# Kernel optimization log

Hardware: AMD Instinct MI355X
Metric: run time of the kernel (lower is better)

Reference implementation:

```python
import jax, jax.numpy as jnp
import numpy as np

N, E, D, C, H1 = 50000, 800000, 128, 8, 2


def setup_inputs() -> dict:
    key = jax.random.key(0)
    ks = jax.random.split(key, 14)
    s = lambda k, sh: (jax.random.normal(k, sh, jnp.float32) * 0.05)
    return {
        "x": jax.random.normal(ks[0], (N, D), jnp.float32),
        "edge_index": jax.random.randint(ks[1], (2, E), 0, N, dtype=jnp.int32),
        # conv1: GATConv(D, D, heads=2, concat=True)
        "W1": s(ks[2], (D, H1 * D)),
        "att1_src": s(ks[3], (H1, D)),
        "att1_dst": s(ks[4], (H1, D)),
        "b1": s(ks[5], (H1 * D,)),
        # conv2: GATConv(2D, D, heads=1, concat=False)
        "W2": s(ks[6], (H1 * D, D)),
        "att2_src": s(ks[7], (1, D)),
        "att2_dst": s(ks[8], (1, D)),
        "b2": s(ks[9], (D,)),
        # MLP head
        "Wm1": s(ks[10], (D, D)),
        "bm1": s(ks[11], (D,)),
        "Wm2": s(ks[12], (D, C)),
        "bm2": s(ks[13], (C,)),
    }


def gat_conv(x, src, dst, W, a_src, a_dst, b, heads, out_ch, concat):
    """PyG GATConv (eval mode): self-loops added by caller, softmax over
    edges grouped by destination node, negative_slope=0.2."""
    n = x.shape[0]
    h = (x @ W).reshape(n, heads, out_ch)              # [N,H,F]
    alpha_src = jnp.einsum('nhf,hf->nh', h, a_src)     # [N,H]
    alpha_dst = jnp.einsum('nhf,hf->nh', h, a_dst)     # [N,H]
    e = jax.nn.leaky_relu(alpha_src[src] + alpha_dst[dst], 0.2)  # [E,H]
    e_max = jax.ops.segment_max(e, dst, num_segments=n)
    ex = jnp.exp(e - e_max[dst])
    denom = jax.ops.segment_sum(ex, dst, num_segments=n)
    alpha = ex / jnp.maximum(denom[dst], 1e-16)        # [E,H]
    out = jax.ops.segment_sum(h[src] * alpha[:, :, None], dst, num_segments=n)
    out = out.reshape(n, heads * out_ch) if concat else out.mean(axis=1)
    return out + b


def reference(x, edge_index, W1, att1_src, att1_dst, b1,
              W2, att2_src, att2_dst, b2, Wm1, bm1, Wm2, bm2):
    n = x.shape[0]
    loop = jnp.arange(n, dtype=edge_index.dtype)
    src = jnp.concatenate([edge_index[0], loop])  # add_self_loops=True
    dst = jnp.concatenate([edge_index[1], loop])
    h = jax.nn.elu(gat_conv(x, src, dst, W1, att1_src, att1_dst, b1, H1, D, True))
    h = jax.nn.elu(gat_conv(h, src, dst, W2, att2_src, att2_dst, b2, 1, D, False))
    h = jax.nn.relu(h @ Wm1 + bm1)
    return jax.nn.relu(h @ Wm2 + bm2)
```

## Files before the change

### kernel.cpp

```cpp
#include <hip/hip_runtime.h>
#include <hip/hip_bf16.h>


__device__ __forceinline__ float lrelu(float x){ return x > 0.f ? x : 0.2f*x; }
__device__ __forceinline__ float elu_f(float x){ return x > 0.f ? x : __expf(x) - 1.f; }
__device__ __forceinline__ unsigned short f2bf(float f){
  __hip_bfloat16 h = __float2bfloat16(f);
  return *reinterpret_cast<unsigned short*>(&h);
}
__device__ __forceinline__ float bflo(unsigned int u){ return __uint_as_float(u << 16); }
__device__ __forceinline__ float bfhi(unsigned int u){ return __uint_as_float(u & 0xffff0000u); }
__device__ __forceinline__ unsigned int packbf(float a, float b){
  return (unsigned int)f2bf(a) | ((unsigned int)f2bf(b) << 16);
}

typedef __attribute__((ext_vector_type(8))) short bf16x8;
typedef __attribute__((ext_vector_type(4))) float f32x4;

__global__ void prep_kernel(const float* __restrict__ W1, unsigned short* __restrict__ BT1a,
                            unsigned short* __restrict__ BT1b,
                            const float* __restrict__ W2, unsigned short* __restrict__ BT2,
                            const float* __restrict__ Wm1, unsigned short* __restrict__ BT3,
                            const float* __restrict__ a1s, const float* __restrict__ a1d,
                            float* __restrict__ va, int* __restrict__ bcount,
                            int* __restrict__ gcur, int NB){
  int idx = blockIdx.x*256 + threadIdx.x;
  const int S1 = 128*256, S2 = 128*256, S3 = 128*128;
  if (idx < S1){
    int k = idx >> 8, c = idx & 255;
    unsigned short v = f2bf(W1[idx]);
    if (c < 128) BT1a[c*128 + k] = v;
    else         BT1b[(c-128)*128 + k] = v;
  } else if (idx < S1 + S2){
    int j = idx - S1;
    int k = j >> 7, n = j & 127;
    BT2[n*256 + k] = f2bf(W2[j]);
  } else if (idx < S1 + S2 + S3){
    int j = idx - S1 - S2;
    int k = j >> 7, n = j & 127;
    BT3[n*128 + k] = f2bf(Wm1[j]);
  } else if (idx < S1 + S2 + S3 + 512){
    int j = idx - S1 - S2 - S3;
    int v = j >> 7, k = j & 127;
    const float* avec = (v < 2) ? a1s : a1d;
    int head = v & 1;
    const float4* wrow = (const float4*)(W1 + (size_t)k*256 + head*128);
    const float4* arow = (const float4*)(avec + head*128);
    float s = 0.f;
    #pragma unroll 8
    for (int f = 0; f < 32; ++f){
      float4 w = wrow[f], a = arow[f];
      s += w.x*a.x + w.y*a.y + w.z*a.z + w.w*a.w;
    }
    va[j] = s;
  } else if (idx < S1 + S2 + S3 + 512 + 2048){
    int z = idx - (S1 + S2 + S3 + 512);
    if (z < 1024){ if (z < NB) bcount[z] = 0; }
    else { z -= 1024; if (z < NB) gcur[z] = 0; }
  }
}

__global__ __launch_bounds__(256) void f2bf_hist_kernel(
    const float* __restrict__ x, unsigned short* __restrict__ xb, int N,
    const float* __restrict__ va, float* __restrict__ as1, float* __restrict__ ad1,
    const int* __restrict__ dst, int E, int* __restrict__ bcount, int NB, int nbConv)
{
  __shared__ int h[1024];
  if ((int)blockIdx.x < nbConv){
    int i = blockIdx.x*256 + threadIdx.x;
    int total = N*32;
    float4 v = make_float4(0.f,0.f,0.f,0.f);
    if (i < total){
      v = ((const float4*)x)[i];
      ushort4 u; u.x=f2bf(v.x); u.y=f2bf(v.y); u.z=f2bf(v.z); u.w=f2bf(v.w);
      ((ushort4*)xb)[i] = u;
    }
    int c = (i & 31) << 2;
    float4 vs0 = *(const float4*)(va + c);
    float4 vs1 = *(const float4*)(va + 128 + c);
    float4 vd0 = *(const float4*)(va + 256 + c);
    float4 vd1 = *(const float4*)(va + 384 + c);
    float s0 = v.x*vs0.x + v.y*vs0.y + v.z*vs0.z + v.w*vs0.w;
    float s1 = v.x*vs1.x + v.y*vs1.y + v.z*vs1.z + v.w*vs1.w;
    float d0 = v.x*vd0.x + v.y*vd0.y + v.z*vd0.z + v.w*vd0.w;
    float d1 = v.x*vd1.x + v.y*vd1.y + v.z*vd1.z + v.w*vd1.w;
    #pragma unroll
    for (int m = 1; m <= 16; m <<= 1){
      s0 += __shfl_xor(s0, m); s1 += __shfl_xor(s1, m);
      d0 += __shfl_xor(d0, m); d1 += __shfl_xor(d1, m);
    }
    if ((i & 31) == 0 && i < total){
      int n = i >> 5;
      *(float2*)(as1 + 2*n) = make_float2(s0, s1);
      *(float2*)(ad1 + 2*n) = make_float2(d0, d1);
    }
  } else {
    for (int i = threadIdx.x; i < NB; i += 256) h[i] = 0;
    __syncthreads();
    int b0 = blockIdx.x - nbConv;
    for (int e = b0*256 + threadIdx.x; e < E; e += 64*256)
      atomicAdd(&h[dst[e] >> 6], 1);
    __syncthreads();
    for (int i = threadIdx.x; i < NB; i += 256)
      if (h[i]) atomicAdd(&bcount[i], h[i]);
  }
}

__global__ __launch_bounds__(256) void bscatter_kernel(
    const int* __restrict__ src, const int* __restrict__ dst, int E,
    const int* __restrict__ bcount, int* __restrict__ boff,
    int* __restrict__ gcur, unsigned int* __restrict__ pairs, int NB)
{
  __shared__ int h[1024];
  __shared__ int runbase[1024];
  __shared__ int sc[1024];
  const int t = threadIdx.x;
  const int e0 = blockIdx.x * 4096;

  for (int i = t; i < 1024; i += 256) sc[i] = (i < NB) ? bcount[i] : 0;
  for (int i = t; i < NB; i += 256) h[i] = 0;
  __syncthreads();
  for (int d = 1; d < 1024; d <<= 1){
    int v0 = (t       >= d) ? sc[t       - d] : 0;
    int v1 = (t + 256 >= d) ? sc[t + 256 - d] : 0;
    int v2 = (t + 512 >= d) ? sc[t + 512 - d] : 0;
    int v3 = (t + 768 >= d) ? sc[t + 768 - d] : 0;
    __syncthreads();
    sc[t] += v0; sc[t+256] += v1; sc[t+512] += v2; sc[t+768] += v3;
    __syncthreads();
  }
  if (blockIdx.x == 0){
    for (int i = t; i <= NB; i += 256) boff[i] = i ? sc[i-1] : 0;
  }

  int myb[16]; unsigned int myw[16];
  #pragma unroll
  for (int q = 0; q < 16; ++q){
    int e = e0 + q*256 + t;
    int b = -1; unsigned int w = 0;
    if (e < E){
      int d = dst[e];
      b = d >> 6;
      w = ((unsigned int)(d & 63) << 26) | (unsigned int)src[e];
      atomicAdd(&h[b], 1);
    }
    myb[q] = b; myw[q] = w;
  }
  __syncthreads();
  for (int i = t; i < NB; i += 256)
    runbase[i] = h[i] ? atomicAdd(&gcur[i], h[i]) : 0;
  __syncthreads();
  for (int i = t; i < NB; i += 256) h[i] = 0;
  __syncthreads();
  #pragma unroll
  for (int q = 0; q < 16; ++q){
    if (myb[q] >= 0){
      int off = atomicAdd(&h[myb[q]], 1);
      int base = myb[q] ? sc[myb[q]-1] : 0;
      pairs[(size_t)base + runbase[myb[q]] + off] = myw[q];
    }
  }
}

__global__ __launch_bounds__(256) void bbuild_kernel(
    const unsigned int* __restrict__ pairs, const int* __restrict__ boff,
    int* __restrict__ rowptr, int* __restrict__ csr, int N)
{
  __shared__ int deg[64], offs[64], cur[64];
  const int b = blockIdx.x;
  const int t = threadIdx.x;
  const int n0 = b << 6;
  const int nNodes = min(64, N - n0);
  const int p0 = boff[b], p1 = boff[b+1];
  const int base = p0 + n0;
  if (t < 64) deg[t] = (t < nNodes) ? 1 : 0;
  __syncthreads();
  for (int i = p0 + t; i < p1; i += 256)
    atomicAdd(&deg[pairs[i] >> 26], 1);
  __syncthreads();
  if (t < 64){
    int x = deg[t];
    #pragma unroll
    for (int d = 1; d < 64; d <<= 1){
      int y = __shfl_up(x, d);
      if (t >= d) x += y;
    }
    offs[t] = x - deg[t];
    cur[t] = 1;
    if (t < nNodes){
      rowptr[n0 + t + 1] = base + x;
      csr[base + x - deg[t]] = n0 + t;
    }
    if (b == 0 && t == 0) rowptr[0] = 0;
  }
  __syncthreads();
  for (int i = p0 + t; i < p1; i += 256){
    unsigned int w = pairs[i];
    int dl = w >> 26;
    int s  = (int)(w & 0x03ffffffu);
    int off = atomicAdd(&cur[dl], 1);
    csr[base + offs[dl] + off] = s;
  }
}

__device__ __forceinline__ void gemm_core(
    const unsigned short* __restrict__ A, int lda,
    const unsigned short* __restrict__ BT, int M, int K, int r0,
    unsigned short* a_s, unsigned short* b_s, f32x4 (&acc)[4][4])
{
  const int tid  = threadIdx.x;
  const int lane = tid & 63, wv = tid >> 6;
  const int mh = (wv & 1)*64, nh = (wv >> 1)*64;
  const int l15 = lane & 15, quad = lane >> 4;
  const int srow = tid >> 3, skc = tid & 7;

  #pragma unroll
  for (int i = 0; i < 4; ++i)
    #pragma unroll
    for (int j = 0; j < 4; ++j)
      #pragma unroll
      for (int r = 0; r < 4; ++r) acc[i][j][r] = 0.f;

  for (int k0 = 0; k0 < K; k0 += 64){
    #pragma unroll
    for (int it = 0; it < 4; ++it){
      int row = it*32 + srow;
      int grow = r0 + row;
      uint4 v = make_uint4(0u,0u,0u,0u);
      if (grow < M) v = *(const uint4*)(A + (size_t)grow*lda + k0 + skc*8);
      *(uint4*)(&a_s[row*72 + skc*8]) = v;
    }
    #pragma unroll
    for (int it = 0; it < 4; ++it){
      int row = it*32 + srow;
      uint4 v = *(const uint4*)(BT + (size_t)row*K + k0 + skc*8);
      *(uint4*)(&b_s[row*72 + skc*8]) = v;
    }
    __syncthreads();
    #pragma unroll
    for (int ks = 0; ks < 64; ks += 32){
      bf16x8 af[4], bfr[4];
      #pragma unroll
      for (int i = 0; i < 4; ++i)
        af[i] = *(const bf16x8*)(&a_s[(mh + i*16 + l15)*72 + ks + quad*8]);
      #pragma unroll
      for (int j = 0; j < 4; ++j)
        bfr[j] = *(const bf16x8*)(&b_s[(nh + j*16 + l15)*72 + ks + quad*8]);
      #pragma unroll
      for (int i = 0; i < 4; ++i)
        #pragma unroll
        for (int j = 0; j < 4; ++j)
          acc[i][j] = __builtin_amdgcn_mfma_f32_16x16x32_bf16(bfr[j], af[i], acc[i][j], 0, 0, 0);
    }
    __syncthreads();
  }
}

__global__ __launch_bounds__(256) void gemm_conv2_kernel(
    const unsigned short* __restrict__ out1b, const unsigned short* __restrict__ BT2,
    unsigned short* __restrict__ h2b, int M,
    const float* __restrict__ a2s, const float* __restrict__ a2d,
    float* __restrict__ as2, float* __restrict__ ad2)
{
  __shared__ unsigned short a_s[128*72];
  __shared__ unsigned short b_s[128*72];
  __shared__ float part_s[128][2];
  __shared__ float part_d[128][2];
  const int r0 = blockIdx.y*128;
  f32x4 acc[4][4];
  gemm_core(out1b, 256, BT2, M, 256, r0, a_s, b_s, acc);

  const int tid = threadIdx.x;
  const int lane = tid & 63, wv = tid >> 6;
  const int mh = (wv & 1)*64, nh = (wv >> 1)*64;
  const int l15 = lane & 15, quad = lane >> 4;
  #pragma unroll
  for (int i = 0; i < 4; ++i){
    int m = r0 + mh + i*16 + l15;
    float ps = 0.f, pd = 0.f;
    #pragma unroll
    for (int j = 0; j < 4; ++j){
      int n = nh + j*16 + quad*4;
      float4 wsv = *(const float4*)(a2s + n);
      float4 wdv = *(const float4*)(a2d + n);
      float v0 = acc[i][j][0], v1 = acc[i][j][1], v2 = acc[i][j][2], v3 = acc[i][j][3];
      ps += v0*wsv.x + v1*wsv.y + v2*wsv.z + v3*wsv.w;
      pd += v0*wdv.x + v1*wdv.y + v2*wdv.z + v3*wdv.w;
      if (m < M){
        ushort4 u;
        u.x = f2bf(v0); u.y = f2bf(v1); u.z = f2bf(v2); u.w = f2bf(v3);
        *(ushort4*)(h2b + (size_t)m*128 + n) = u;
      }
    }
    ps += __shfl_xor(ps, 16); ps += __shfl_xor(ps, 32);
    pd += __shfl_xor(pd, 16); pd += __shfl_xor(pd, 32);
    if (quad == 0){
      part_s[mh + i*16 + l15][wv >> 1] = ps;
      part_d[mh + i*16 + l15][wv >> 1] = pd;
    }
  }
  __syncthreads();
  if (tid < 128){
    int gm = r0 + tid;
    if (gm < M){
      as2[gm] = part_s[tid][0] + part_s[tid][1];
      ad2[gm] = part_d[tid][0] + part_d[tid][1];
    }
  }
}

#define AGG1_FMA(u, a0v, a1v) do{ \
    float f0 = bflo(u.x), f1 = bfhi(u.x), f2v = bflo(u.y), f3 = bfhi(u.y); \
    float f4 = bflo(u.z), f5 = bfhi(u.z), f6 = bflo(u.w), f7 = bfhi(u.w); \
    acc0[0] += a0v*f0; acc0[1] += a0v*f1; acc0[2] += a0v*f2v; acc0[3] += a0v*f3; \
    acc0[4] += a0v*f4; acc0[5] += a0v*f5; acc0[6] += a0v*f6;  acc0[7] += a0v*f7; \
    acc1[0] += a1v*f0; acc1[1] += a1v*f1; acc1[2] += a1v*f2v; acc1[3] += a1v*f3; \
    acc1[4] += a1v*f4; acc1[5] += a1v*f5; acc1[6] += a1v*f6;  acc1[7] += a1v*f7; \
  }while(0)

#define AGG2_FMA(u, av) do{ \
    acc[0] += av*bflo(u.x); acc[1] += av*bfhi(u.x); \
    acc[2] += av*bflo(u.y); acc[3] += av*bfhi(u.y); \
    acc[4] += av*bflo(u.z); acc[5] += av*bfhi(u.z); \
    acc[6] += av*bflo(u.w); acc[7] += av*bfhi(u.w); \
  }while(0)

__global__ __launch_bounds__(256, 4) void agg1gemm_kernel(
    const unsigned short* __restrict__ xb, const float* __restrict__ as_,
    const float* __restrict__ ad_, const int* __restrict__ rowptr, const int* __restrict__ csr,
    const unsigned short* __restrict__ BT1a, const unsigned short* __restrict__ BT1b,
    const float* __restrict__ b1, unsigned short* __restrict__ out1b, int N)
{
  __shared__ unsigned short xa_s[16*264];
  const int tid = threadIdx.x;
  const int wv = tid >> 6, lane = tid & 63;
  const int ql = lane & 15;
  const int g = wv*4 + (lane >> 4);
  const int n = blockIdx.x*16 + g;
  const bool valid = n < N;
  int start = 0, end = 0;
  float2 adv = make_float2(0.f, 0.f);
  if (valid){ start = rowptr[n]; end = rowptr[n+1]; adv = *(const float2*)(ad_ + 2*n); }

  int jl = start + ql;
  bool have = valid && (jl < end);
  int s_l = 0;
  float p0 = 0.f, p1 = 0.f;
  if (have){
    s_l = csr[jl];
    float2 av = *(const float2*)(as_ + 2*s_l);
    p0 = __expf(lrelu(av.x + adv.x));
    p1 = __expf(lrelu(av.y + adv.y));
  }
  float l0 = p0, l1 = p1;
  for (int j = jl + 16; j < end; j += 16){
    int s = csr[j];
    float2 av = *(const float2*)(as_ + 2*s);
    l0 += __expf(lrelu(av.x + adv.x));
    l1 += __expf(lrelu(av.y + adv.y));
  }
  #pragma unroll
  for (int msk = 1; msk <= 8; msk <<= 1){
    l0 += __shfl_xor(l0, msk);
    l1 += __shfl_xor(l1, msk);
  }
  float inv0 = 1.f / fmaxf(l0, 1e-16f);
  float inv1 = 1.f / fmaxf(l1, 1e-16f);
  float a0_l = p0 * inv0;
  float a1_l = p1 * inv1;

  float acc0[8], acc1[8];
  #pragma unroll
  for (int i = 0; i < 8; ++i){ acc0[i] = 0.f; acc1[i] = 0.f; }
  const int c = ql << 3;
  const unsigned short* hp = xb + c;

  #pragma unroll
  for (int t = 0; t < 16; t += 2){
    int   sA  = __shfl(s_l, t, 16),   sB  = __shfl(s_l, t+1, 16);
    float a0A = __shfl(a0_l, t, 16),  a0B = __shfl(a0_l, t+1, 16);
    float a1A = __shfl(a1_l, t, 16),  a1B = __shfl(a1_l, t+1, 16);
    uint4 uA = *(const uint4*)(hp + (sA << 7));
    uint4 uB = *(const uint4*)(hp + (sB << 7));
    AGG1_FMA(uA, a0A, a1A);
    AGG1_FMA(uB, a0B, a1B);
  }
  for (int jb = start + 16; jb < end; jb += 16){
    int jl2 = jb + ql;
    int s2 = 0; float a0_2 = 0.f, a1_2 = 0.f;
    if (jl2 < end){
      s2 = csr[jl2];
      float2 av = *(const float2*)(as_ + 2*s2);
      a0_2 = __expf(lrelu(av.x + adv.x)) * inv0;
      a1_2 = __expf(lrelu(av.y + adv.y)) * inv1;
    }
    int cnt2 = min(16, end - jb);
    for (int t2 = 0; t2 < cnt2; t2 += 2){
      int   sA  = __shfl(s2, t2, 16),   sB  = __shfl(s2, t2+1, 16);
      float a0A = __shfl(a0_2, t2, 16), a0B = __shfl(a0_2, t2+1, 16);
      float a1A = __shfl(a1_2, t2, 16), a1B = __shfl(a1_2, t2+1, 16);
      uint4 uA = *(const uint4*)(hp + (sA << 7));
      uint4 uB = *(const uint4*)(hp + (sB << 7));
      AGG1_FMA(uA, a0A, a1A);
      AGG1_FMA(uB, a0B, a1B);
    }
  }

  {
    uint4 u0, u1;
    u0.x = packbf(acc0[0], acc0[1]); u0.y = packbf(acc0[2], acc0[3]);
    u0.z = packbf(acc0[4], acc0[5]); u0.w = packbf(acc0[6], acc0[7]);
    u1.x = packbf(acc1[0], acc1[1]); u1.y = packbf(acc1[2], acc1[3]);
    u1.z = packbf(acc1[4], acc1[5]); u1.w = packbf(acc1[6], acc1[7]);
    *(uint4*)(&xa_s[g*264 + c])       = u0;
    *(uint4*)(&xa_s[g*264 + 128 + c]) = u1;
  }
  __syncthreads();

  const int h = wv >> 1;
  const int colbase = (wv & 1)*64;
  const unsigned short* BT = (h ? BT1b : BT1a) + (size_t)colbase*128;
  const int l15 = lane & 15, quad = lane >> 4;
  f32x4 acc[4];
  #pragma unroll
  for (int j = 0; j < 4; ++j)
    #pragma unroll
    for (int r = 0; r < 4; ++r) acc[j][r] = 0.f;

  #pragma unroll
  for (int ks = 0; ks < 128; ks += 32){
    bf16x8 af = *(const bf16x8*)(&xa_s[l15*264 + h*128 + ks + quad*8]);
    #pragma unroll
    for (int j = 0; j < 4; ++j){
      bf16x8 bfr = *(const bf16x8*)(BT + (size_t)(j*16 + l15)*128 + ks + quad*8);
      acc[j] = __builtin_amdgcn_mfma_f32_16x16x32_bf16(bfr, af, acc[j], 0, 0, 0);
    }
  }

  const int m = blockIdx.x*16 + l15;
  if (m < N){
    const float* bias = b1 + h*128 + colbase;
    #pragma unroll
    for (int j = 0; j < 4; ++j){
      int nn = j*16 + quad*4;
      float4 bb = *(const float4*)(bias + nn);
      ushort4 u;
      u.x = f2bf(elu_f(acc[j][0] + bb.x));
      u.y = f2bf(elu_f(acc[j][1] + bb.y));
      u.z = f2bf(elu_f(acc[j][2] + bb.z));
      u.w = f2bf(elu_f(acc[j][3] + bb.w));
      *(ushort4*)(out1b + (size_t)m*256 + h*128 + colbase + nn) = u;
    }
  }
}

__global__ __launch_bounds__(256, 4) void agg2mlp_kernel(
    const unsigned short* __restrict__ h2b, const float* __restrict__ as_,
    const float* __restrict__ ad_, const int* __restrict__ rowptr, const int* __restrict__ csr,
    const float* __restrict__ b2, const unsigned short* __restrict__ BT3,
    const float* __restrict__ bm1, const float* __restrict__ Wm2,
    const float* __restrict__ bm2, float* __restrict__ out, int N)
{
  __shared__ unsigned short gb_s[16*136];
  __shared__ float wm2_s[128*8];
  __shared__ float part[16][4][8];
  const int tid = threadIdx.x;
  {
    int i4 = tid*4;
    *(float4*)(&wm2_s[i4]) = *(const float4*)(Wm2 + i4);
  }
  const int wv = tid >> 6, lane = tid & 63;
  const int ql = lane & 15;
  const int g = wv*4 + (lane >> 4);
  const int n = blockIdx.x*16 + g;
  const bool valid = n < N;
  int start = 0, end = 0;
  float adn = 0.f;
  if (valid){ start = rowptr[n]; end = rowptr[n+1]; adn = ad_[n]; }

  int jl = start + ql;
  bool have = valid && (jl < end);
  int s_l = 0;
  float p_l = 0.f;
  if (have){
    s_l = csr[jl];
    p_l = __expf(lrelu(as_[s_l] + adn));
  }
  float l = p_l;
  for (int j = jl + 16; j < end; j += 16)
    l += __expf(lrelu(as_[csr[j]] + adn));
  #pragma unroll
  for (int msk = 1; msk <= 8; msk <<= 1) l += __shfl_xor(l, msk);
  float inv = 1.f / fmaxf(l, 1e-16f);
  float a_l = p_l * inv;

  float acc[8];
  #pragma unroll
  for (int i = 0; i < 8; ++i) acc[i] = 0.f;
  const int c = ql << 3;
  const unsigned short* hp = h2b + c;

  #pragma unroll
  for (int t = 0; t < 16; t += 2){
    int   sA = __shfl(s_l, t, 16),  sB = __shfl(s_l, t+1, 16);
    float aA = __shfl(a_l, t, 16),  aB = __shfl(a_l, t+1, 16);
    uint4 uA = *(const uint4*)(hp + (sA << 7));
    uint4 uB = *(const uint4*)(hp + (sB << 7));
    AGG2_FMA(uA, aA);
    AGG2_FMA(uB, aB);
  }
  for (int jb = start + 16; jb < end; jb += 16){
    int jl2 = jb + ql;
    int s2 = 0; float a2 = 0.f;
    if (jl2 < end){
      s2 = csr[jl2];
      a2 = __expf(lrelu(as_[s2] + adn)) * inv;
    }
    int cnt2 = min(16, end - jb);
    for (int t2 = 0; t2 < cnt2; t2 += 2){
      int   sA = __shfl(s2, t2, 16),  sB = __shfl(s2, t2+1, 16);
      float aA = __shfl(a2, t2, 16),  aB = __shfl(a2, t2+1, 16);
      uint4 uA = *(const uint4*)(hp + (sA << 7));
      uint4 uB = *(const uint4*)(hp + (sB << 7));
      AGG2_FMA(uA, aA);
      AGG2_FMA(uB, aB);
    }
  }

  {
    float4 bb0 = *(const float4*)(b2 + c);
    float4 bb1 = *(const float4*)(b2 + c + 4);
    float o[8];
    o[0]=elu_f(acc[0]+bb0.x); o[1]=elu_f(acc[1]+bb0.y);
    o[2]=elu_f(acc[2]+bb0.z); o[3]=elu_f(acc[3]+bb0.w);
    o[4]=elu_f(acc[4]+bb1.x); o[5]=elu_f(acc[5]+bb1.y);
    o[6]=elu_f(acc[6]+bb1.z); o[7]=elu_f(acc[7]+bb1.w);
    uint4 up;
    up.x = packbf(o[0], o[1]); up.y = packbf(o[2], o[3]);
    up.z = packbf(o[4], o[5]); up.w = packbf(o[6], o[7]);
    *(uint4*)(&gb_s[g*136 + c]) = up;
  }
  __syncthreads();

  const int l15 = lane & 15, quad = lane >> 4;
  const int nh = wv*32;
  f32x4 macc[2];
  #pragma unroll
  for (int j = 0; j < 2; ++j)
    #pragma unroll
    for (int r = 0; r < 4; ++r) macc[j][r] = 0.f;

  #pragma unroll
  for (int ks = 0; ks < 128; ks += 32){
    bf16x8 af = *(const bf16x8*)(&gb_s[l15*136 + ks + quad*8]);
    #pragma unroll
    for (int j = 0; j < 2; ++j){
      bf16x8 bfr = *(const bf16x8*)(BT3 + (size_t)(nh + j*16 + l15)*128 + ks + quad*8);
      macc[j] = __builtin_amdgcn_mfma_f32_16x16x32_bf16(bfr, af, macc[j], 0, 0, 0);
    }
  }

  float po[8];
  #pragma unroll
  for (int o = 0; o < 8; ++o) po[o] = 0.f;
  #pragma unroll
  for (int j = 0; j < 2; ++j){
    int nn = nh + j*16 + quad*4;
    float4 bb = *(const float4*)(bm1 + nn);
    #pragma unroll
    for (int r = 0; r < 4; ++r){
      float hcol = fmaxf(macc[j][r] + ((const float*)&bb)[r], 0.f);
      const float* wr = &wm2_s[(nn + r)*8];
      #pragma unroll
      for (int o = 0; o < 8; ++o) po[o] += hcol*wr[o];
    }
  }
  #pragma unroll
  for (int o = 0; o < 8; ++o){
    po[o] += __shfl_xor(po[o], 16);
    po[o] += __shfl_xor(po[o], 32);
  }
  if (quad == 0){
    #pragma unroll
    for (int o = 0; o < 8; ++o) part[l15][wv][o] = po[o];
  }
  __syncthreads();
  if (tid < 16){
    int gm = blockIdx.x*16 + tid;
    if (gm < N){
      float4 o0, o1;
      o0.x = fmaxf(part[tid][0][0]+part[tid][1][0]+part[tid][2][0]+part[tid][3][0] + bm2[0], 0.f);
      o0.y = fmaxf(part[tid][0][1]+part[tid][1][1]+part[tid][2][1]+part[tid][3][1] + bm2[1], 0.f);
      o0.z = fmaxf(part[tid][0][2]+part[tid][1][2]+part[tid][2][2]+part[tid][3][2] + bm2[2], 0.f);
      o0.w = fmaxf(part[tid][0][3]+part[tid][1][3]+part[tid][2][3]+part[tid][3][3] + bm2[3], 0.f);
      o1.x = fmaxf(part[tid][0][4]+part[tid][1][4]+part[tid][2][4]+part[tid][3][4] + bm2[4], 0.f);
      o1.y = fmaxf(part[tid][0][5]+part[tid][1][5]+part[tid][2][5]+part[tid][3][5] + bm2[5], 0.f);
      o1.z = fmaxf(part[tid][0][6]+part[tid][1][6]+part[tid][2][6]+part[tid][3][6] + bm2[6], 0.f);
      o1.w = fmaxf(part[tid][0][7]+part[tid][1][7]+part[tid][2][7]+part[tid][3][7] + bm2[7], 0.f);
      *(float4*)(out + (size_t)gm*8)     = o0;
      *(float4*)(out + (size_t)gm*8 + 4) = o1;
    }
  }
}

extern "C" void kernel_launch(void* const* d_in, const int* in_sizes, int n_in,
                              void* d_out, int out_size, void* d_ws, size_t ws_size,
                              hipStream_t stream)
{
  (void)n_in; (void)out_size; (void)ws_size;
  const float* x   = (const float*)d_in[0];
  const int*   ei  = (const int*)d_in[1];
  const float* W1  = (const float*)d_in[2];
  const float* a1s = (const float*)d_in[3];
  const float* a1d = (const float*)d_in[4];
  const float* b1  = (const float*)d_in[5];
  const float* W2  = (const float*)d_in[6];
  const float* a2s = (const float*)d_in[7];
  const float* a2d = (const float*)d_in[8];
  const float* b2  = (const float*)d_in[9];
  const float* Wm1 = (const float*)d_in[10];
  const float* bm1 = (const float*)d_in[11];
  const float* Wm2 = (const float*)d_in[12];
  const float* bm2 = (const float*)d_in[13];
  float* out = (float*)d_out;

  const int N = in_sizes[0] / 128;
  const int E = in_sizes[1] / 2;
  const int NB = (N + 63) >> 6;
  const int* srcp = ei;
  const int* dstp = ei + E;

  char* ws = (char*)d_ws;
  unsigned short* xb    = (unsigned short*)ws;
  unsigned short* out1b = (unsigned short*)(ws + (size_t)N*256);
  unsigned short* h2b   = (unsigned short*)(ws + (size_t)N*768);
  char* tail = ws + (size_t)N*1024;
  unsigned short* BT1a = (unsigned short*)tail;
  unsigned short* BT1b = BT1a + 128*128;
  unsigned short* BT2  = BT1b + 128*128;
  unsigned short* BT3  = BT2 + 128*256;
  float* va   = (float*)(BT3 + 128*128);
  float* as1  = va + 512;
  float* ad1  = as1 + (size_t)2*N;
  float* as2  = ad1 + (size_t)2*N;
  float* ad2  = as2 + N;
  int* bcount = (int*)(ad2 + N);
  int* boff   = bcount + 1024;
  int* gcur   = boff + 1032;
  int* rowptr = gcur + 1024;
  int* csr    = rowptr + N + 1;
  unsigned int* pairs = (unsigned int*)(csr + E + N);

  const int nbConv = (N*32 + 255)/256;
  const int prepTotal = 128*256 + 128*256 + 128*128 + 512 + 2048;

  prep_kernel<<<(prepTotal + 255)/256, 256, 0, stream>>>(
      W1, BT1a, BT1b, W2, BT2, Wm1, BT3, a1s, a1d, va, bcount, gcur, NB);
  f2bf_hist_kernel<<<nbConv + 64, 256, 0, stream>>>(x, xb, N, va, as1, ad1,
                                                    dstp, E, bcount, NB, nbConv);
  bscatter_kernel<<<(E + 4095)/4096, 256, 0, stream>>>(srcp, dstp, E, bcount, boff, gcur, pairs, NB);
  bbuild_kernel<<<NB, 256, 0, stream>>>(pairs, boff, rowptr, csr, N);

  const int nb16 = (N + 15) / 16;
  const int gy   = (N + 127) / 128;

  agg1gemm_kernel<<<nb16, 256, 0, stream>>>(xb, as1, ad1, rowptr, csr,
                                            BT1a, BT1b, b1, out1b, N);
  gemm_conv2_kernel<<<dim3(1, gy), 256, 0, stream>>>(out1b, BT2, h2b, N, a2s, a2d, as2, ad2);
  agg2mlp_kernel<<<nb16, 256, 0, stream>>>(h2b, as2, ad2, rowptr, csr,
                                           b2, BT3, bm1, Wm2, bm2, out, N);
}
```

Baseline: 267.1 us.

## Make aggregation+GEMM per-wave independent, removing block barriers

Both fused aggregation kernels now give each wave its own 8 nodes, processed in two passes, and a private LDS tile, so each wave runs its MFMA GEMM without a block-wide __syncthreads. Each block covers 32 nodes instead of 16, and the second kernel drops its cross-wave partial-sum reduction through shared memory. The cost is that half of the 16 MFMA rows are wasted and each wave now loads the full weight matrix instead of a slice, which raises weight traffic and MFMA work per node.

```diff
diff --git a/kernel.cpp b/kernel.cpp
--- a/kernel.cpp
+++ b/kernel.cpp
@@ -331,125 +331,127 @@
     const unsigned short* __restrict__ BT1a, const unsigned short* __restrict__ BT1b,
     const float* __restrict__ b1, unsigned short* __restrict__ out1b, int N)
 {
-  __shared__ unsigned short xa_s[16*264];
+  __shared__ unsigned short xa_s[4][8*264];
   const int tid = threadIdx.x;
   const int wv = tid >> 6, lane = tid & 63;
   const int ql = lane & 15;
-  const int g = wv*4 + (lane >> 4);
-  const int n = blockIdx.x*16 + g;
-  const bool valid = n < N;
-  int start = 0, end = 0;
-  float2 adv = make_float2(0.f, 0.f);
-  if (valid){ start = rowptr[n]; end = rowptr[n+1]; adv = *(const float2*)(ad_ + 2*n); }
-
-  int jl = start + ql;
-  bool have = valid && (jl < end);
-  int s_l = 0;
-  float p0 = 0.f, p1 = 0.f;
-  if (have){
-    s_l = csr[jl];
-    float2 av = *(const float2*)(as_ + 2*s_l);
-    p0 = __expf(lrelu(av.x + adv.x));
-    p1 = __expf(lrelu(av.y + adv.y));
-  }
-  float l0 = p0, l1 = p1;
-  for (int j = jl + 16; j < end; j += 16){
-    int s = csr[j];
-    float2 av = *(const float2*)(as_ + 2*s);
-    l0 += __expf(lrelu(av.x + adv.x));
-    l1 += __expf(lrelu(av.y + adv.y));
-  }
-  #pragma unroll
-  for (int msk = 1; msk <= 8; msk <<= 1){
-    l0 += __shfl_xor(l0, msk);
-    l1 += __shfl_xor(l1, msk);
-  }
-  float inv0 = 1.f / fmaxf(l0, 1e-16f);
-  float inv1 = 1.f / fmaxf(l1, 1e-16f);
-  float a0_l = p0 * inv0;
-  float a1_l = p1 * inv1;
-
-  float acc0[8], acc1[8];
-  #pragma unroll
-  for (int i = 0; i < 8; ++i){ acc0[i] = 0.f; acc1[i] = 0.f; }
   const int c = ql << 3;
   const unsigned short* hp = xb + c;
-
-  #pragma unroll
-  for (int t = 0; t < 16; t += 2){
-    int   sA  = __shfl(s_l, t, 16),   sB  = __shfl(s_l, t+1, 16);
-    float a0A = __shfl(a0_l, t, 16),  a0B = __shfl(a0_l, t+1, 16);
-    float a1A = __shfl(a1_l, t, 16),  a1B = __shfl(a1_l, t+1, 16);
-    uint4 uA = *(const uint4*)(hp + (sA << 7));
-    uint4 uB = *(const uint4*)(hp + (sB << 7));
-    AGG1_FMA(uA, a0A, a1A);
-    AGG1_FMA(uB, a0B, a1B);
-  }
-  for (int jb = start + 16; jb < end; jb += 16){
-    int jl2 = jb + ql;
-    int s2 = 0; float a0_2 = 0.f, a1_2 = 0.f;
-    if (jl2 < end){
-      s2 = csr[jl2];
-      float2 av = *(const float2*)(as_ + 2*s2);
-      a0_2 = __expf(lrelu(av.x + adv.x)) * inv0;
-      a1_2 = __expf(lrelu(av.y + adv.y)) * inv1;
-    }
-    int cnt2 = min(16, end - jb);
-    for (int t2 = 0; t2 < cnt2; t2 += 2){
-      int   sA  = __shfl(s2, t2, 16),   sB  = __shfl(s2, t2+1, 16);
-      float a0A = __shfl(a0_2, t2, 16), a0B = __shfl(a0_2, t2+1, 16);
-      float a1A = __shfl(a1_2, t2, 16), a1B = __shfl(a1_2, t2+1, 16);
+  unsigned short* xs = &xa_s[wv][0];
+  const int nodebase = blockIdx.x*32 + wv*8;
+
+  for (int pass = 0; pass < 2; ++pass){
+    const int row = pass*4 + (lane >> 4);
+    const int n = nodebase + row;
+    const bool valid = n < N;
+    int start = 0, end = 0;
+    float2 adv = make_float2(0.f, 0.f);
+    if (valid){ start = rowptr[n]; end = rowptr[n+1]; adv = *(const float2*)(ad_ + 2*n); }
+
+    int jl = start + ql;
+    bool have = valid && (jl < end);
+    int s_l = 0;
+    float p0 = 0.f, p1 = 0.f;
+    if (have){
+      s_l = csr[jl];
+      float2 av = *(const float2*)(as_ + 2*s_l);
+      p0 = __expf(lrelu(av.x + adv.x));
+      p1 = __expf(lrelu(av.y + adv.y));
+    }
+    float l0 = p0, l1 = p1;
+    for (int j = jl + 16; j < end; j += 16){
+      int s = csr[j];
+      float2 av = *(const float2*)(as_ + 2*s);
+      l0 += __expf(lrelu(av.x + adv.x));
+      l1 += __expf(lrelu(av.y + adv.y));
+    }
+    #pragma unroll
+    for (int msk = 1; msk <= 8; msk <<= 1){
+      l0 += __shfl_xor(l0, msk);
+      l1 += __shfl_xor(l1, msk);
+    }
+    float inv0 = 1.f / fmaxf(l0, 1e-16f);
+    float inv1 = 1.f / fmaxf(l1, 1e-16f);
+    float a0_l = p0 * inv0;
+    float a1_l = p1 * inv1;
+
+    float acc0[8], acc1[8];
+    #pragma unroll
+    for (int i = 0; i < 8; ++i){ acc0[i] = 0.f; acc1[i] = 0.f; }
+
+    #pragma unroll
+    for (int t = 0; t < 16; t += 2){
+      int   sA  = __shfl(s_l, t, 16),   sB  = __shfl(s_l, t+1, 16);
+      float a0A = __shfl(a0_l, t, 16),  a0B = __shfl(a0_l, t+1, 16);
+      float a1A = __shfl(a1_l, t, 16),  a1B = __shfl(a1_l, t+1, 16);
       uint4 uA = *(const uint4*)(hp + (sA << 7));
       uint4 uB = *(const uint4*)(hp + (sB << 7));
       AGG1_FMA(uA, a0A, a1A);
       AGG1_FMA(uB, a0B, a1B);
     }
-  }
-
-  {
+    for (int jb = start + 16; jb < end; jb += 16){
+      int jl2 = jb + ql;
+      int s2 = 0; float a0_2 = 0.f, a1_2 = 0.f;
+      if (jl2 < end){
+        s2 = csr[jl2];
+        float2 av = *(const float2*)(as_ + 2*s2);
+        a0_2 = __expf(lrelu(av.x + adv.x)) * inv0;
+        a1_2 = __expf(lrelu(av.y + adv.y)) * inv1;
+      }
+      int cnt2 = min(16, end - jb);
+      for (int t2 = 0; t2 < cnt2; t2 += 2){
+        int   sA  = __shfl(s2, t2, 16),   sB  = __shfl(s2, t2+1, 16);
+        float a0A = __shfl(a0_2, t2, 16), a0B = __shfl(a0_2, t2+1, 16);
+        float a1A = __shfl(a1_2, t2, 16), a1B = __shfl(a1_2, t2+1, 16);
+        uint4 uA = *(const uint4*)(hp + (sA << 7));
+        uint4 uB = *(const uint4*)(hp + (sB << 7));
+        AGG1_FMA(uA, a0A, a1A);
+        AGG1_FMA(uB, a0B, a1B);
+      }
+    }
+
     uint4 u0, u1;
     u0.x = packbf(acc0[0], acc0[1]); u0.y = packbf(acc0[2], acc0[3]);
     u0.z = packbf(acc0[4], acc0[5]); u0.w = packbf(acc0[6], acc0[7]);
     u1.x = packbf(acc1[0], acc1[1]); u1.y = packbf(acc1[2], acc1[3]);
     u1.z = packbf(acc1[4], acc1[5]); u1.w = packbf(acc1[6], acc1[7]);
-    *(uint4*)(&xa_s[g*264 + c])       = u0;
-    *(uint4*)(&xa_s[g*264 + 128 + c]) = u1;
-  }
-  __syncthreads();
-
-  const int h = wv >> 1;
-  const int colbase = (wv & 1)*64;
-  const unsigned short* BT = (h ? BT1b : BT1a) + (size_t)colbase*128;
+    *(uint4*)(&xs[row*264 + c])       = u0;
+    *(uint4*)(&xs[row*264 + 128 + c]) = u1;
+  }
+  asm volatile("" ::: "memory");
+
   const int l15 = lane & 15, quad = lane >> 4;
-  f32x4 acc[4];
-  #pragma unroll
-  for (int j = 0; j < 4; ++j)
-    #pragma unroll
-    for (int r = 0; r < 4; ++r) acc[j][r] = 0.f;
-
-  #pragma unroll
-  for (int ks = 0; ks < 128; ks += 32){
-    bf16x8 af = *(const bf16x8*)(&xa_s[l15*264 + h*128 + ks + quad*8]);
-    #pragma unroll
-    for (int j = 0; j < 4; ++j){
-      bf16x8 bfr = *(const bf16x8*)(BT + (size_t)(j*16 + l15)*128 + ks + quad*8);
-      acc[j] = __builtin_amdgcn_mfma_f32_16x16x32_bf16(bfr, af, acc[j], 0, 0, 0);
-    }
-  }
-
-  const int m = blockIdx.x*16 + l15;
-  if (m < N){
-    const float* bias = b1 + h*128 + colbase;
-    #pragma unroll
-    for (int j = 0; j < 4; ++j){
-      int nn = j*16 + quad*4;
-      float4 bb = *(const float4*)(bias + nn);
-      ushort4 u;
-      u.x = f2bf(elu_f(acc[j][0] + bb.x));
-      u.y = f2bf(elu_f(acc[j][1] + bb.y));
-      u.z = f2bf(elu_f(acc[j][2] + bb.z));
-      u.w = f2bf(elu_f(acc[j][3] + bb.w));
-      *(ushort4*)(out1b + (size_t)m*256 + h*128 + colbase + nn) = u;
+  const int arow = l15 & 7;
+  const int m = nodebase + l15;
+  const bool mok = (l15 < 8) && (m < N);
+  #pragma unroll
+  for (int h = 0; h < 2; ++h){
+    bf16x8 af[4];
+    #pragma unroll
+    for (int k = 0; k < 4; ++k)
+      af[k] = *(const bf16x8*)(&xs[arow*264 + h*128 + k*32 + quad*8]);
+    const unsigned short* BT = h ? BT1b : BT1a;
+    const float* bias = b1 + h*128;
+    #pragma unroll
+    for (int j = 0; j < 8; ++j){
+      f32x4 acc;
+      #pragma unroll
+      for (int r = 0; r < 4; ++r) acc[r] = 0.f;
+      #pragma unroll
+      for (int k = 0; k < 4; ++k){
+        bf16x8 bfr = *(const bf16x8*)(BT + (size_t)(j*16 + l15)*128 + k*32 + quad*8);
+        acc = __builtin_amdgcn_mfma_f32_16x16x32_bf16(bfr, af[k], acc, 0, 0, 0);
+      }
+      if (mok){
+        int nn = j*16 + quad*4;
+        float4 bb = *(const float4*)(bias + nn);
+        ushort4 u;
+        u.x = f2bf(elu_f(acc[0] + bb.x));
+        u.y = f2bf(elu_f(acc[1] + bb.y));
+        u.z = f2bf(elu_f(acc[2] + bb.z));
+        u.w = f2bf(elu_f(acc[3] + bb.w));
+        *(ushort4*)(out1b + (size_t)m*256 + h*128 + nn) = u;
+      }
     }
   }
 }
@@ -461,73 +463,77 @@
     const float* __restrict__ bm1, const float* __restrict__ Wm2,
     const float* __restrict__ bm2, float* __restrict__ out, int N)
 {
-  __shared__ unsigned short gb_s[16*136];
+  __shared__ unsigned short gb_s[4][8*136];
   __shared__ float wm2_s[128*8];
-  __shared__ float part[16][4][8];
   const int tid = threadIdx.x;
   {
     int i4 = tid*4;
     *(float4*)(&wm2_s[i4]) = *(const float4*)(Wm2 + i4);
   }
+  __syncthreads();
+
   const int wv = tid >> 6, lane = tid & 63;
   const int ql = lane & 15;
-  const int g = wv*4 + (lane >> 4);
-  const int n = blockIdx.x*16 + g;
-  const bool valid = n < N;
-  int start = 0, end = 0;
-  float adn = 0.f;
-  if (valid){ start = rowptr[n]; end = rowptr[n+1]; adn = ad_[n]; }
-
-  int jl = start + ql;
-  bool have = valid && (jl < end);
-  int s_l = 0;
-  float p_l = 0.f;
-  if (have){
-    s_l = csr[jl];
-    p_l = __expf(lrelu(as_[s_l] + adn));
-  }
-  float l = p_l;
-  for (int j = jl + 16; j < end; j += 16)
-    l += __expf(lrelu(as_[csr[j]] + adn));
-  #pragma unroll
-  for (int msk = 1; msk <= 8; msk <<= 1) l += __shfl_xor(l, msk);
-  float inv = 1.f / fmaxf(l, 1e-16f);
-  float a_l = p_l * inv;
-
-  float acc[8];
-  #pragma unroll
-  for (int i = 0; i < 8; ++i) acc[i] = 0.f;
   const int c = ql << 3;
   const unsigned short* hp = h2b + c;
-
-  #pragma unroll
-  for (int t = 0; t < 16; t += 2){
-    int   sA = __shfl(s_l, t, 16),  sB = __shfl(s_l, t+1, 16);
-    float aA = __shfl(a_l, t, 16),  aB = __shfl(a_l, t+1, 16);
-    uint4 uA = *(const uint4*)(hp + (sA << 7));
-    uint4 uB = *(const uint4*)(hp + (sB << 7));
-    AGG2_FMA(uA, aA);
-    AGG2_FMA(uB, aB);
-  }
-  for (int jb = start + 16; jb < end; jb += 16){
-    int jl2 = jb + ql;
-    int s2 = 0; float a2 = 0.f;
-    if (jl2 < end){
-      s2 = csr[jl2];
-      a2 = __expf(lrelu(as_[s2] + adn)) * inv;
-    }
-    int cnt2 = min(16, end - jb);
-    for (int t2 = 0; t2 < cnt2; t2 += 2){
-      int   sA = __shfl(s2, t2, 16),  sB = __shfl(s2, t2+1, 16);
-      float aA = __shfl(a2, t2, 16),  aB = __shfl(a2, t2+1, 16);
+  unsigned short* gs = &gb_s[wv][0];
+  const int nodebase = blockIdx.x*32 + wv*8;
+
+  for (int pass = 0; pass < 2; ++pass){
+    const int row = pass*4 + (lane >> 4);
+    const int n = nodebase + row;
+    const bool valid = n < N;
+    int start = 0, end = 0;
+    float adn = 0.f;
+    if (valid){ start = rowptr[n]; end = rowptr[n+1]; adn = ad_[n]; }
+
+    int jl = start + ql;
+    bool have = valid && (jl < end);
+    int s_l = 0;
+    float p_l = 0.f;
+    if (have){
+      s_l = csr[jl];
+      p_l = __expf(lrelu(as_[s_l] + adn));
+    }
+    float l = p_l;
+    for (int j = jl + 16; j < end; j += 16)
+      l += __expf(lrelu(as_[csr[j]] + adn));
+    #pragma unroll
+    for (int msk = 1; msk <= 8; msk <<= 1) l += __shfl_xor(l, msk);
+    float inv = 1.f / fmaxf(l, 1e-16f);
+    float a_l = p_l * inv;
+
+    float acc[8];
+    #pragma unroll
+    for (int i = 0; i < 8; ++i) acc[i] = 0.f;
+
+    #pragma unroll
+    for (int t = 0; t < 16; t += 2){
+      int   sA = __shfl(s_l, t, 16),  sB = __shfl(s_l, t+1, 16);
+      float aA = __shfl(a_l, t, 16),  aB = __shfl(a_l, t+1, 16);
       uint4 uA = *(const uint4*)(hp + (sA << 7));
       uint4 uB = *(const uint4*)(hp + (sB << 7));
       AGG2_FMA(uA, aA);
       AGG2_FMA(uB, aB);
     }
-  }
-
-  {
+    for (int jb = start + 16; jb < end; jb += 16){
+      int jl2 = jb + ql;
+      int s2 = 0; float a2 = 0.f;
+      if (jl2 < end){
+        s2 = csr[jl2];
+        a2 = __expf(lrelu(as_[s2] + adn)) * inv;
+      }
+      int cnt2 = min(16, end - jb);
+      for (int t2 = 0; t2 < cnt2; t2 += 2){
+        int   sA = __shfl(s2, t2, 16),  sB = __shfl(s2, t2+1, 16);
+        float aA = __shfl(a2, t2, 16),  aB = __shfl(a2, t2+1, 16);
+        uint4 uA = *(const uint4*)(hp + (sA << 7));
+        uint4 uB = *(const uint4*)(hp + (sB << 7));
+        AGG2_FMA(uA, aA);
+        AGG2_FMA(uB, aB);
+      }
+    }
+
     float4 bb0 = *(const float4*)(b2 + c);
     float4 bb1 = *(const float4*)(b2 + c + 4);
     float o[8];
@@ -538,38 +544,35 @@
     uint4 up;
     up.x = packbf(o[0], o[1]); up.y = packbf(o[2], o[3]);
     up.z = packbf(o[4], o[5]); up.w = packbf(o[6], o[7]);
-    *(uint4*)(&gb_s[g*136 + c]) = up;
-  }
-  __syncthreads();
+    *(uint4*)(&gs[row*136 + c]) = up;
+  }
+  asm volatile("" ::: "memory");
 
   const int l15 = lane & 15, quad = lane >> 4;
-  const int nh = wv*32;
-  f32x4 macc[2];
-  #pragma unroll
-  for (int j = 0; j < 2; ++j)
-    #pragma unroll
-    for (int r = 0; r < 4; ++r) macc[j][r] = 0.f;
-
-  #pragma unroll
-  for (int ks = 0; ks < 128; ks += 32){
-    bf16x8 af = *(const bf16x8*)(&gb_s[l15*136 + ks + quad*8]);
-    #pragma unroll
-    for (int j = 0; j < 2; ++j){
-      bf16x8 bfr = *(const bf16x8*)(BT3 + (size_t)(nh + j*16 + l15)*128 + ks + quad*8);
-      macc[j] = __builtin_amdgcn_mfma_f32_16x16x32_bf16(bfr, af, macc[j], 0, 0, 0);
-    }
-  }
+  const int arow = l15 & 7;
+  bf16x8 af[4];
+  #pragma unroll
+  for (int k = 0; k < 4; ++k)
+    af[k] = *(const bf16x8*)(&gs[arow*136 + k*32 + quad*8]);
 
   float po[8];
   #pragma unroll
   for (int o = 0; o < 8; ++o) po[o] = 0.f;
   #pragma unroll
-  for (int j = 0; j < 2; ++j){
-    int nn = nh + j*16 + quad*4;
+  for (int j = 0; j < 8; ++j){
+    f32x4 acc;
+    #pragma unroll
+    for (int r = 0; r < 4; ++r) acc[r] = 0.f;
+    #pragma unroll
+    for (int k = 0; k < 4; ++k){
+      bf16x8 bfr = *(const bf16x8*)(BT3 + (size_t)(j*16 + l15)*128 + k*32 + quad*8);
+      acc = __builtin_amdgcn_mfma_f32_16x16x32_bf16(bfr, af[k], acc, 0, 0, 0);
+    }
+    int nn = j*16 + quad*4;
     float4 bb = *(const float4*)(bm1 + nn);
     #pragma unroll
     for (int r = 0; r < 4; ++r){
-      float hcol = fmaxf(macc[j][r] + ((const float*)&bb)[r], 0.f);
+      float hcol = fmaxf(acc[r] + ((const float*)&bb)[r], 0.f);
       const float* wr = &wm2_s[(nn + r)*8];
       #pragma unroll
       for (int o = 0; o < 8; ++o) po[o] += hcol*wr[o];
@@ -580,23 +583,18 @@
     po[o] += __shfl_xor(po[o], 16);
     po[o] += __shfl_xor(po[o], 32);
   }
-  if (quad == 0){
-    #pragma unroll
-    for (int o = 0; o < 8; ++o) part[l15][wv][o] = po[o];
-  }
-  __syncthreads();
-  if (tid < 16){
-    int gm = blockIdx.x*16 + tid;
+  if (quad == 0 && l15 < 8){
+    int gm = nodebase + l15;
     if (gm < N){
       float4 o0, o1;
-      o0.x = fmaxf(part[tid][0][0]+part[tid][1][0]+part[tid][2][0]+part[tid][3][0] + bm2[0], 0.f);
-      o0.y = fmaxf(part[tid][0][1]+part[tid][1][1]+part[tid][2][1]+part[tid][3][1] + bm2[1], 0.f);
-      o0.z = fmaxf(part[tid][0][2]+part[tid][1][2]+part[tid][2][2]+part[tid][3][2] + bm2[2], 0.f);
-      o0.w = fmaxf(part[tid][0][3]+part[tid][1][3]+part[tid][2][3]+part[tid][3][3] + bm2[3], 0.f);
-      o1.x = fmaxf(part[tid][0][4]+part[tid][1][4]+part[tid][2][4]+part[tid][3][4] + bm2[4], 0.f);
-      o1.y = fmaxf(part[tid][0][5]+part[tid][1][5]+part[tid][2][5]+part[tid][3][5] + bm2[5], 0.f);
-      o1.z = fmaxf(part[tid][0][6]+part[tid][1][6]+part[tid][2][6]+part[tid][3][6] + bm2[6], 0.f);
-      o1.w = fmaxf(part[tid][0][7]+part[tid][1][7]+part[tid][2][7]+part[tid][3][7] + bm2[7], 0.f);
+      o0.x = fmaxf(po[0] + bm2[0], 0.f);
+      o0.y = fmaxf(po[1] + bm2[1], 0.f);
+      o0.z = fmaxf(po[2] + bm2[2], 0.f);
+      o0.w = fmaxf(po[3] + bm2[3], 0.f);
+      o1.x = fmaxf(po[4] + bm2[4], 0.f);
+      o1.y = fmaxf(po[5] + bm2[5], 0.f);
+      o1.z = fmaxf(po[6] + bm2[6], 0.f);
+      o1.w = fmaxf(po[7] + bm2[7], 0.f);
       *(float4*)(out + (size_t)gm*8)     = o0;
       *(float4*)(out + (size_t)gm*8 + 4) = o1;
     }
@@ -661,12 +659,12 @@
   bscatter_kernel<<<(E + 4095)/4096, 256, 0, stream>>>(srcp, dstp, E, bcount, boff, gcur, pairs, NB);
   bbuild_kernel<<<NB, 256, 0, stream>>>(pairs, boff, rowptr, csr, N);
 
-  const int nb16 = (N + 15) / 16;
+  const int nb32 = (N + 31) / 32;
   const int gy   = (N + 127) / 128;
 
-  agg1gemm_kernel<<<nb16, 256, 0, stream>>>(xb, as1, ad1, rowptr, csr,
+  agg1gemm_kernel<<<nb32, 256, 0, stream>>>(xb, as1, ad1, rowptr, csr,
                                             BT1a, BT1b, b1, out1b, N);
   gemm_conv2_kernel<<<dim3(1, gy), 256, 0, stream>>>(out1b, BT2, h2b, N, a2s, a2d, as2, ad2);
-  agg2mlp_kernel<<<nb16, 256, 0, stream>>>(h2b, as2, ad2, rowptr, csr,
+  agg2mlp_kernel<<<nb32, 256, 0, stream>>>(h2b, as2, ad2, rowptr, csr,
                                            b2, BT3, bm1, Wm2, bm2, out, N);
 }
```

After: 306.0 us. 14.6% more time.
